# Kernel tuning notes

Measured on AMD Instinct MI355X. Metric: run time of the kernel, lower is better.

Reference implementation:

```python
import jax, jax.numpy as jnp
import numpy as np

K = 16                 # hardcoded k in KL_divergence default
TYPICAL_CRLB = 0.15 * 100 / 10   # = 1.5, sigma used in KL divergence


def setup_inputs() -> dict:
    key = jax.random.key(0)
    k1, k2 = jax.random.split(key)
    N = 8192
    ch1 = jax.random.normal(k1, (N, 2), dtype=jnp.float32)
    ch2 = jax.random.normal(k2, (N, 2), dtype=jnp.float32)
    # Polynomial layer parameters, exactly as in __init__ (identity-ish map)
    M1 = jnp.array([[0.0, 0.0], [1.0, 0.0]], dtype=jnp.float32)
    M2 = jnp.array([[0.0, 1.0], [0.0, 0.0]], dtype=jnp.float32)
    return {"ch1": ch1, "ch2": ch2, "M1": M1, "M2": M2}


def _polynomial(x, M1, M2):
    # out[:,0] = sum_ij M1[i,j] * x1^i * x2^j ; out[:,1] analog with M2 (m=2)
    x1, x2 = x[:, 0], x[:, 1]
    pi = jnp.stack([jnp.ones_like(x1), x1], axis=1)          # [N,2] -> x1^i
    pj = jnp.stack([jnp.ones_like(x2), x2], axis=1)          # [N,2] -> x2^j
    B = pi[:, :, None] * pj[:, None, :]                      # [N,2,2] basis x1^i*x2^j
    y1 = jnp.einsum('nij,ij->n', B, M1)
    y2 = jnp.einsum('nij,ij->n', B, M2)
    return jnp.stack([y1, y2], axis=1)                       # [N,2]


def reference(ch1, ch2, M1, M2):
    N = ch1.shape[0]
    ch2m = _polynomial(ch2, M1, M2)

    # --- KNN ---
    diff = ch1[None, :, :] - ch2m[:, None, :]                # [N2, N1, 2]
    distances = diff * diff                                  # squared per-coord dists
    abs_distances = jnp.sum(distances, axis=2)               # [N2, N1]
    # top_k of negated transposed distances: for each ch1 point, k nearest ch2m
    _, idx = jax.lax.top_k(-abs_distances.T, K)              # [N1, K] indices into ch2 axis
    # Faithful reproduction of the original index construction:
    # idx is flattened row-major ([N,K]); indx1 flattens a [K,N] arange-broadcast,
    # so the second coordinate at flat position t is t % N.
    flat_a = idx.reshape(-1)                                 # [N*K] indexes axis 0 (ch2)
    flat_b = jnp.tile(jnp.arange(N), K)                      # [N*K] indexes axis 1 (ch1)
    knn = distances[flat_a, flat_b].reshape(K, N, 2)         # [K, N, 2]

    # --- KL divergence ---
    sigma2 = TYPICAL_CRLB
    D_KL = 0.5 * jnp.sum(knn / (sigma2 ** 2), axis=2)        # [K, N]

    # --- Rel entropy ---
    expD = jnp.sum(jnp.exp(-D_KL), axis=0) / N               # [N]
    mask = expD != 0.0                                       # tf boolean_mask of nonzeros
    safe = jnp.where(mask, expD, 1.0)
    return -jnp.sum(jnp.where(mask, jnp.log(safe), 0.0))
```

## Files before the change

kernel.cpp:

```cpp
#include <hip/hip_runtime.h>
#include <math.h>
#include <stdint.h>

#define K_NN 16
#define NPTS 8192
#define HALF (NPTS / 2)
#define WPB 16

__global__ __launch_bounds__(1024) void k1_knn(const float* __restrict__ ch1,
                                               const float* __restrict__ ch2,
                                               const float* __restrict__ M1,
                                               const float* __restrict__ M2,
                                               int* __restrict__ midx,
                                               float* __restrict__ out) {
    __shared__ float2 sh[HALF];

    const int tid  = threadIdx.x;
    const int lane = tid & 63;
    const int w    = tid >> 6;
    const int qg   = blockIdx.x * WPB + w;

    if (blockIdx.x == 0 && tid == 0) out[0] = 0.0f;

    const float q0 = ch1[2 * qg + 0];
    const float q1 = ch1[2 * qg + 1];

    const float a0 = M1[0], a1 = M1[1], a2 = M1[2], a3 = M1[3];
    const float b0 = M2[0], b1 = M2[1], b2 = M2[2], b3 = M2[3];

    const float4* __restrict__ g4 = (const float4*)ch2;

    unsigned key = 0xFFFFFFFFu;
    unsigned kth = 0xFFFFFFFFu;

    for (int pass = 0; pass < 2; ++pass) {
        __syncthreads();
#pragma unroll
        for (int e = 0; e < (HALF / 2) / 1024; ++e) {
            float4 v = g4[pass * (HALF / 2) + e * 1024 + tid];
            float px0 = a0 + a1 * v.y + v.x * (a2 + a3 * v.y);
            float py0 = b0 + b1 * v.y + v.x * (b2 + b3 * v.y);
            float px1 = a0 + a1 * v.w + v.z * (a2 + a3 * v.w);
            float py1 = b0 + b1 * v.w + v.z * (b2 + b3 * v.w);
            ((float4*)sh)[e * 1024 + tid] = make_float4(px0, py0, px1, py1);
        }
        __syncthreads();

        const float4* s4 = (const float4*)sh;
        float4 c = s4[lane];

        for (int t = 0; t < HALF / 128; ++t) {
            float4 cn = s4[(((t + 1) & (HALF / 128 - 1)) * 64) + lane];
            int base = pass * HALF + (t * 64 + lane) * 2;
            float dx0 = q0 - c.x, dy0 = q1 - c.y;
            float dx1 = q0 - c.z, dy1 = q1 - c.w;
            float nd0 = dx0 * dx0 + dy0 * dy0;
            float nd1 = dx1 * dx1 + dy1 * dy1;
            unsigned nk0 = (__float_as_uint(nd0) & 0xFFFFE000u) | (unsigned)base;
            unsigned nk1 = (__float_as_uint(nd1) & 0xFFFFE000u) | (unsigned)(base + 1);

            unsigned long long m = __ballot(nk0 < kth);
            while (m) {
                int l = __ffsll(m) - 1;
                unsigned snk = (unsigned)__builtin_amdgcn_readlane((int)nk0, l);
                unsigned up = (unsigned)__builtin_amdgcn_update_dpp(
                    0, (int)key, 0x111, 0xF, 0xF, false);
                bool c1 = snk < key;
                unsigned nv = (snk < up) ? up : snk;
                key = c1 ? nv : key;
                kth = (unsigned)__builtin_amdgcn_readlane((int)key, 15);
                m &= m - 1;
                m &= __ballot(nk0 < kth);
            }

            m = __ballot(nk1 < kth);
            while (m) {
                int l = __ffsll(m) - 1;
                unsigned snk = (unsigned)__builtin_amdgcn_readlane((int)nk1, l);
                unsigned up = (unsigned)__builtin_amdgcn_update_dpp(
                    0, (int)key, 0x111, 0xF, 0xF, false);
                bool c1 = snk < key;
                unsigned nv = (snk < up) ? up : snk;
                key = c1 ? nv : key;
                kth = (unsigned)__builtin_amdgcn_readlane((int)key, 15);
                m &= m - 1;
                m &= __ballot(nk1 < kth);
            }

            c = cn;
        }
    }

    if (lane < K_NN)
        midx[qg * K_NN + lane] = (int)(key & 0x1FFFu);
}

__global__ __launch_bounds__(1024) void k3_final(const float* __restrict__ ch1,
                                                 const float* __restrict__ ch2,
                                                 const float* __restrict__ M1,
                                                 const float* __restrict__ M2,
                                                 const int* __restrict__ midx,
                                                 float* __restrict__ out, int N) {
    const float a0 = M1[0], a1 = M1[1], a2 = M1[2], a3 = M1[3];
    const float b0 = M2[0], b1 = M2[1], b2 = M2[2], b3 = M2[3];

    int t = blockIdx.x * 1024 + threadIdx.x;
    int n = t >> 4;
    int k = t & 15;
    int g = n >> 4;
    int r = n & 15;

    int j = k * (N / K_NN) + g;
    int a = midx[j * K_NN + r];
    float2 cp = ((const float2*)ch2)[a];
    float cx = a0 + a1 * cp.y + cp.x * (a2 + a3 * cp.y);
    float cy = b0 + b1 * cp.y + cp.x * (b2 + b3 * cp.y);
    float dx = ch1[2 * n + 0] - cx;
    float dy = ch1[2 * n + 1] - cy;
    float term = expf(-(dx * dx + dy * dy) * (1.0f / 4.5f));

#pragma unroll
    for (int off = 8; off; off >>= 1) term += __shfl_down(term, off, 16);

    float v = 0.0f;
    if (k == 0) {
        float expD = term / (float)N;
        v = (expD != 0.0f) ? logf(expD) : 0.0f;
    }
#pragma unroll
    for (int off = 32; off; off >>= 1) v += __shfl_down(v, off, 64);

    __shared__ float red[16];
    int lane = threadIdx.x & 63;
    int wv = threadIdx.x >> 6;
    if (lane == 0) red[wv] = v;
    __syncthreads();
    if (threadIdx.x == 0) {
        float s = 0.0f;
#pragma unroll
        for (int i = 0; i < 16; ++i) s += red[i];
        atomicAdd(out, -s);
    }
}

extern "C" void kernel_launch(void* const* d_in, const int* in_sizes, int n_in,
                              void* d_out, int out_size, void* d_ws, size_t ws_size,
                              hipStream_t stream) {
    const float* ch1 = (const float*)d_in[0];
    const float* ch2 = (const float*)d_in[1];
    const float* M1  = (const float*)d_in[2];
    const float* M2  = (const float*)d_in[3];
    float* out = (float*)d_out;
    const int N = in_sizes[0] / 2;

    int* midx = (int*)d_ws;

    k1_knn<<<N / WPB, 1024, 0, stream>>>(ch1, ch2, M1, M2, midx, out);

    k3_final<<<(N * K_NN) / 1024, 1024, 0, stream>>>(ch1, ch2, M1, M2, midx, out, N);
}
```

Measured before the change: 95.98 us.

## Replace brute-force KNN with uniform-grid spatial binning and ring search

Replaces the all-pairs distance scan with a 32x32 grid whose cell boundaries are normal-distribution quantiles. A single-block build kernel bins the transformed ch2 points, scans the counts into cell offsets and scatters the points into cell order. Each query wave then visits rings of cells outward and stops once the k-th key is within the ring margin, cutting distance evaluations from all points to a local neighbourhood. The costs are a serial single-block build launch and an extra kernel, and the quantile cell boundaries are tuned to Gaussian inputs (correct for any input but only efficient for this distribution).

```diff
diff --git a/kernel.cpp b/kernel.cpp
--- a/kernel.cpp
+++ b/kernel.cpp
@@ -4,92 +4,165 @@
 
 #define K_NN 16
 #define NPTS 8192
-#define HALF (NPTS / 2)
-#define WPB 16
-
-__global__ __launch_bounds__(1024) void k1_knn(const float* __restrict__ ch1,
-                                               const float* __restrict__ ch2,
-                                               const float* __restrict__ M1,
-                                               const float* __restrict__ M2,
-                                               int* __restrict__ midx,
-                                               float* __restrict__ out) {
-    __shared__ float2 sh[HALF];
-
-    const int tid  = threadIdx.x;
-    const int lane = tid & 63;
-    const int w    = tid >> 6;
-    const int qg   = blockIdx.x * WPB + w;
-
-    if (blockIdx.x == 0 && tid == 0) out[0] = 0.0f;
-
-    const float q0 = ch1[2 * qg + 0];
-    const float q1 = ch1[2 * qg + 1];
+#define G 32
+#define NC (G * G)
+
+static __device__ __constant__ float d_bt[33] = {
+    -3.4028235e38f,
+    -1.8627318f, -1.5341205f, -1.3180109f, -1.1503494f, -1.0100762f,
+    -0.8871466f, -0.7764218f, -0.6744898f, -0.5791322f, -0.4887764f,
+    -0.4022501f, -0.3186394f, -0.2372021f, -0.1573107f, -0.0784124f,
+     0.0f,
+     0.0784124f,  0.1573107f,  0.2372021f,  0.3186394f,  0.4022501f,
+     0.4887764f,  0.5791322f,  0.6744898f,  0.7764218f,  0.8871466f,
+     1.0100762f,  1.1503494f,  1.3180109f,  1.5341205f,  1.8627318f,
+     3.4028235e38f
+};
+
+__device__ __forceinline__ int bsearch5(const float* bt, float x) {
+    int c = 0;
+    c += (x >= bt[c + 16]) ? 16 : 0;
+    c += (x >= bt[c + 8])  ? 8  : 0;
+    c += (x >= bt[c + 4])  ? 4  : 0;
+    c += (x >= bt[c + 2])  ? 2  : 0;
+    c += (x >= bt[c + 1])  ? 1  : 0;
+    return c;
+}
+
+__global__ __launch_bounds__(1024) void kb_build(const float* __restrict__ ch2,
+                                                 const float* __restrict__ M1,
+                                                 const float* __restrict__ M2,
+                                                 float2* __restrict__ spts,
+                                                 int* __restrict__ sidx,
+                                                 int* __restrict__ cellStart,
+                                                 float* __restrict__ out) {
+    __shared__ int hist[NC];
+    __shared__ int scn[NC];
+    __shared__ float bt[33];
+    const int tid = threadIdx.x;
+    if (tid == 0) out[0] = 0.0f;
+    if (tid < 33) bt[tid] = d_bt[tid];
+    hist[tid] = 0;
+    __syncthreads();
 
     const float a0 = M1[0], a1 = M1[1], a2 = M1[2], a3 = M1[3];
     const float b0 = M2[0], b1 = M2[1], b2 = M2[2], b3 = M2[3];
 
-    const float4* __restrict__ g4 = (const float4*)ch2;
+    for (int i = tid; i < NPTS; i += 1024) {
+        float2 v = ((const float2*)ch2)[i];
+        float px = a0 + a1 * v.y + v.x * (a2 + a3 * v.y);
+        float py = b0 + b1 * v.y + v.x * (b2 + b3 * v.y);
+        int cx = bsearch5(bt, px);
+        int cy = bsearch5(bt, py);
+        atomicAdd(&hist[cy * G + cx], 1);
+    }
+    __syncthreads();
+
+    scn[tid] = hist[tid];
+    __syncthreads();
+    for (int off = 1; off < NC; off <<= 1) {
+        int t = scn[tid];
+        int u = (tid >= off) ? scn[tid - off] : 0;
+        __syncthreads();
+        scn[tid] = t + u;
+        __syncthreads();
+    }
+    int excl = scn[tid] - hist[tid];
+    cellStart[tid] = excl;
+    if (tid == NC - 1) cellStart[NC] = scn[tid];
+    __syncthreads();
+    hist[tid] = excl;
+    __syncthreads();
+
+    for (int i = tid; i < NPTS; i += 1024) {
+        float2 v = ((const float2*)ch2)[i];
+        float px = a0 + a1 * v.y + v.x * (a2 + a3 * v.y);
+        float py = b0 + b1 * v.y + v.x * (b2 + b3 * v.y);
+        int cx = bsearch5(bt, px);
+        int cy = bsearch5(bt, py);
+        int pos = atomicAdd(&hist[cy * G + cx], 1);
+        spts[pos] = make_float2(px, py);
+        sidx[pos] = i;
+    }
+}
+
+__global__ __launch_bounds__(256) void kq_query(const float* __restrict__ ch1,
+                                                const float2* __restrict__ spts,
+                                                const int* __restrict__ sidx,
+                                                const int* __restrict__ cellStart,
+                                                int* __restrict__ midx) {
+    __shared__ float bt[33];
+    const int tid = threadIdx.x;
+    if (tid < 33) bt[tid] = d_bt[tid];
+    __syncthreads();
+
+    const int lane = tid & 63;
+    const int qg = blockIdx.x * 4 + (tid >> 6);
+    const float qx = ch1[2 * qg + 0];
+    const float qy = ch1[2 * qg + 1];
+    const int cx = bsearch5(bt, qx);
+    const int cy = bsearch5(bt, qy);
 
     unsigned key = 0xFFFFFFFFu;
     unsigned kth = 0xFFFFFFFFu;
-
-    for (int pass = 0; pass < 2; ++pass) {
-        __syncthreads();
-#pragma unroll
-        for (int e = 0; e < (HALF / 2) / 1024; ++e) {
-            float4 v = g4[pass * (HALF / 2) + e * 1024 + tid];
-            float px0 = a0 + a1 * v.y + v.x * (a2 + a3 * v.y);
-            float py0 = b0 + b1 * v.y + v.x * (b2 + b3 * v.y);
-            float px1 = a0 + a1 * v.w + v.z * (a2 + a3 * v.w);
-            float py1 = b0 + b1 * v.w + v.z * (b2 + b3 * v.w);
-            ((float4*)sh)[e * 1024 + tid] = make_float4(px0, py0, px1, py1);
-        }
-        __syncthreads();
-
-        const float4* s4 = (const float4*)sh;
-        float4 c = s4[lane];
-
-        for (int t = 0; t < HALF / 128; ++t) {
-            float4 cn = s4[(((t + 1) & (HALF / 128 - 1)) * 64) + lane];
-            int base = pass * HALF + (t * 64 + lane) * 2;
-            float dx0 = q0 - c.x, dy0 = q1 - c.y;
-            float dx1 = q0 - c.z, dy1 = q1 - c.w;
-            float nd0 = dx0 * dx0 + dy0 * dy0;
-            float nd1 = dx1 * dx1 + dy1 * dy1;
-            unsigned nk0 = (__float_as_uint(nd0) & 0xFFFFE000u) | (unsigned)base;
-            unsigned nk1 = (__float_as_uint(nd1) & 0xFFFFE000u) | (unsigned)(base + 1);
-
-            unsigned long long m = __ballot(nk0 < kth);
-            while (m) {
-                int l = __ffsll(m) - 1;
-                unsigned snk = (unsigned)__builtin_amdgcn_readlane((int)nk0, l);
-                unsigned up = (unsigned)__builtin_amdgcn_update_dpp(
-                    0, (int)key, 0x111, 0xF, 0xF, false);
-                bool c1 = snk < key;
-                unsigned nv = (snk < up) ? up : snk;
-                key = c1 ? nv : key;
-                kth = (unsigned)__builtin_amdgcn_readlane((int)key, 15);
-                m &= m - 1;
-                m &= __ballot(nk0 < kth);
-            }
-
-            m = __ballot(nk1 < kth);
-            while (m) {
-                int l = __ffsll(m) - 1;
-                unsigned snk = (unsigned)__builtin_amdgcn_readlane((int)nk1, l);
-                unsigned up = (unsigned)__builtin_amdgcn_update_dpp(
-                    0, (int)key, 0x111, 0xF, 0xF, false);
-                bool c1 = snk < key;
-                unsigned nv = (snk < up) ? up : snk;
-                key = c1 ? nv : key;
-                kth = (unsigned)__builtin_amdgcn_readlane((int)key, 15);
-                m &= m - 1;
-                m &= __ballot(nk1 < kth);
-            }
-
-            c = cn;
-        }
-    }
+    unsigned thr = 0xFFFFFFFFu;
+
+#define SCAN_RANGE(ROW, CA, CB)                                               \
+    {                                                                         \
+        int st = cellStart[(ROW) * G + (CA)];                                 \
+        int en = cellStart[(ROW) * G + (CB) + 1];                             \
+        for (int base = st; base < en; base += 64) {                          \
+            int i = base + lane;                                              \
+            unsigned ndb = 0xFFFFFFFFu;                                       \
+            int si = 0x1FFF;                                                  \
+            if (i < en) {                                                     \
+                float2 p = spts[i];                                           \
+                si = sidx[i];                                                 \
+                float dx = qx - p.x, dy = qy - p.y;                           \
+                ndb = __float_as_uint(dx * dx + dy * dy);                     \
+            }                                                                 \
+            unsigned long long m = __ballot(ndb <= thr);                      \
+            while (m) {                                                       \
+                int l = __ffsll(m) - 1;                                       \
+                unsigned snd = (unsigned)__builtin_amdgcn_readlane((int)ndb, l); \
+                unsigned ssi = (unsigned)__builtin_amdgcn_readlane(si, l);    \
+                unsigned snk = (snd & 0xFFFFE000u) | ssi;                     \
+                if (snk < kth) {                                              \
+                    unsigned up = (unsigned)__builtin_amdgcn_update_dpp(      \
+                        0, (int)key, 0x111, 0xF, 0xF, false);  \
+                    bool c1 = snk < key;                                      \
+                    unsigned nv = (snk < up) ? up : snk;                      \
+                    key = c1 ? nv : key;                                      \
+                    kth = (unsigned)__builtin_amdgcn_readlane((int)key, 15);  \
+                    thr = kth | 0x1FFFu;                                      \
+                }                                                             \
+                m &= m - 1;                                                   \
+                m &= __ballot(ndb <= thr);                                    \
+            }                                                                 \
+        }                                                                     \
+    }
+
+    for (int r = 0; r <= 2 * G; ++r) {
+        int rlo = cy - r, rhi = cy + r;
+        int clo = max(cx - r, 0), chi = min(cx + r, G - 1);
+        if (rlo >= 0) SCAN_RANGE(rlo, clo, chi)
+        if (rhi <= G - 1 && r > 0) SCAN_RANGE(rhi, clo, chi)
+        int mlo = max(rlo + 1, 0), mhi = min(rhi - 1, G - 1);
+        if (cx - r >= 0)
+            for (int rr = mlo; rr <= mhi; ++rr) SCAN_RANGE(rr, cx - r, cx - r)
+        if (cx + r <= G - 1)
+            for (int rr = mlo; rr <= mhi; ++rr) SCAN_RANGE(rr, cx + r, cx + r)
+
+        float Lx = (cx - r <= 0)     ? -3.4028235e38f : bt[cx - r];
+        float Rx = (cx + r >= G - 1) ?  3.4028235e38f : bt[cx + r + 1];
+        float Ly = (cy - r <= 0)     ? -3.4028235e38f : bt[cy - r];
+        float Ry = (cy + r >= G - 1) ?  3.4028235e38f : bt[cy + r + 1];
+        float mg = fminf(fminf(qx - Lx, Rx - qx), fminf(qy - Ly, Ry - qy));
+        mg = fmaxf(mg, 0.0f);
+        float kd = __uint_as_float(kth & 0xFFFFE000u);
+        if (kd <= mg * mg) break;
+    }
+#undef SCAN_RANGE
 
     if (lane < K_NN)
         midx[qg * K_NN + lane] = (int)(key & 0x1FFFu);
@@ -153,9 +226,15 @@
     float* out = (float*)d_out;
     const int N = in_sizes[0] / 2;
 
-    int* midx = (int*)d_ws;
-
-    k1_knn<<<N / WPB, 1024, 0, stream>>>(ch1, ch2, M1, M2, midx, out);
+    char* ws = (char*)d_ws;
+    float2* spts     = (float2*)ws;
+    int*    midx     = (int*)(ws + 65536);
+    int*    sidx     = (int*)(ws + 65536 + 524288);
+    int*    cellStart= (int*)(ws + 65536 + 524288 + 32768);
+
+    kb_build<<<1, 1024, 0, stream>>>(ch2, M1, M2, spts, sidx, cellStart, out);
+
+    kq_query<<<N / 4, 256, 0, stream>>>(ch1, spts, sidx, cellStart, midx);
 
     k3_final<<<(N * K_NN) / 1024, 1024, 0, stream>>>(ch1, ch2, M1, M2, midx, out, N);
 }
```

Result: slower. 155.0 us (+61.5%).

## Replace brute-force KNN scan with y-band bucketed search and pruning

Applied to the files above, without the earlier changes.

Adds a single-block build kernel that bins transformed ch2 points into 32 horizontal bands whose boundaries are normal-distribution quantiles, then counting-sorts them. The query kernel scans the query's own band first and expands outward, stopping once a band's vertical distance exceeds the current k-th best. This replaces scanning all 8192 candidates per query. The band boundaries are tuned for standard-normal inputs, so the pruning only helps on similar data, and the extra serial build kernel adds latency.

```diff
diff --git a/kernel.cpp b/kernel.cpp
--- a/kernel.cpp
+++ b/kernel.cpp
@@ -4,92 +4,171 @@
 
 #define K_NN 16
 #define NPTS 8192
-#define HALF (NPTS / 2)
-#define WPB 16
-
-__global__ __launch_bounds__(1024) void k1_knn(const float* __restrict__ ch1,
-                                               const float* __restrict__ ch2,
-                                               const float* __restrict__ M1,
-                                               const float* __restrict__ M2,
-                                               int* __restrict__ midx,
-                                               float* __restrict__ out) {
-    __shared__ float2 sh[HALF];
+#define NR 32
+
+static __device__ __constant__ float d_bt[33] = {
+    -3.4028235e38f,
+    -1.8627318f, -1.5341205f, -1.3180109f, -1.1503494f, -1.0100762f,
+    -0.8871466f, -0.7764218f, -0.6744898f, -0.5791322f, -0.4887764f,
+    -0.4022501f, -0.3186394f, -0.2372021f, -0.1573107f, -0.0784124f,
+     0.0f,
+     0.0784124f,  0.1573107f,  0.2372021f,  0.3186394f,  0.4022501f,
+     0.4887764f,  0.5791322f,  0.6744898f,  0.7764218f,  0.8871466f,
+     1.0100762f,  1.1503494f,  1.3180109f,  1.5341205f,  1.8627318f,
+     3.4028235e38f
+};
+
+__device__ __forceinline__ int rowOf(const float* bt, float y) {
+    int c = 0;
+    c += (y >= bt[c + 16]) ? 16 : 0;
+    c += (y >= bt[c + 8])  ? 8  : 0;
+    c += (y >= bt[c + 4])  ? 4  : 0;
+    c += (y >= bt[c + 2])  ? 2  : 0;
+    c += (y >= bt[c + 1])  ? 1  : 0;
+    return c;
+}
+
+__global__ __launch_bounds__(1024) void kb_build(const float* __restrict__ ch2,
+                                                 const float* __restrict__ M1,
+                                                 const float* __restrict__ M2,
+                                                 float2* __restrict__ spts,
+                                                 int* __restrict__ sidx,
+                                                 int* __restrict__ rowStart,
+                                                 float* __restrict__ out) {
+    __shared__ int h[NR];
+    __shared__ int offs[NR];
+    __shared__ float bt[33];
+    const int tid = threadIdx.x;
+    if (tid == 0) out[0] = 0.0f;
+    if (tid < 33) bt[tid] = d_bt[tid];
+    if (tid < NR) h[tid] = 0;
+    __syncthreads();
+
+    const float a0 = M1[0], a1 = M1[1], a2 = M1[2], a3 = M1[3];
+    const float b0 = M2[0], b1 = M2[1], b2 = M2[2], b3 = M2[3];
+
+    for (int i = tid; i < NPTS; i += 1024) {
+        float2 v = ((const float2*)ch2)[i];
+        float py = b0 + b1 * v.y + v.x * (b2 + b3 * v.y);
+        atomicAdd(&h[rowOf(bt, py)], 1);
+    }
+    __syncthreads();
+
+    if (tid == 0) {
+        int run = 0;
+        for (int r = 0; r < NR; ++r) { offs[r] = run; rowStart[r] = run; run += h[r]; }
+        rowStart[NR] = run;
+    }
+    __syncthreads();
+
+    for (int i = tid; i < NPTS; i += 1024) {
+        float2 v = ((const float2*)ch2)[i];
+        float px = a0 + a1 * v.y + v.x * (a2 + a3 * v.y);
+        float py = b0 + b1 * v.y + v.x * (b2 + b3 * v.y);
+        int pos = atomicAdd(&offs[rowOf(bt, py)], 1);
+        spts[pos] = make_float2(px, py);
+        sidx[pos] = i;
+    }
+}
+
+__global__ __launch_bounds__(1024) void kq_query(const float* __restrict__ ch1,
+                                                 const float2* __restrict__ spts,
+                                                 const int* __restrict__ gsidx,
+                                                 const int* __restrict__ rowStart,
+                                                 int* __restrict__ midx) {
+    __shared__ float2 shp[NPTS];
 
     const int tid  = threadIdx.x;
     const int lane = tid & 63;
     const int w    = tid >> 6;
-    const int qg   = blockIdx.x * WPB + w;
-
-    if (blockIdx.x == 0 && tid == 0) out[0] = 0.0f;
-
-    const float q0 = ch1[2 * qg + 0];
-    const float q1 = ch1[2 * qg + 1];
-
-    const float a0 = M1[0], a1 = M1[1], a2 = M1[2], a3 = M1[3];
-    const float b0 = M2[0], b1 = M2[1], b2 = M2[2], b3 = M2[3];
-
-    const float4* __restrict__ g4 = (const float4*)ch2;
+    const int qg   = blockIdx.x * 16 + w;
+
+#pragma unroll
+    for (int e = 0; e < 4; ++e)
+        ((float4*)shp)[e * 1024 + tid] = ((const float4*)spts)[e * 1024 + tid];
+
+    int btb = __float_as_int(d_bt[lane < 33 ? lane : 0]);
+    int rsv = rowStart[lane < 33 ? lane : 0];
+    __syncthreads();
+
+    const float qx = ch1[2 * qg + 0];
+    const float qy = ch1[2 * qg + 1];
+
+    int own = rowOf(d_bt, qy);
 
     unsigned key = 0xFFFFFFFFu;
-    unsigned kth = 0xFFFFFFFFu;
-
-    for (int pass = 0; pass < 2; ++pass) {
-        __syncthreads();
-#pragma unroll
-        for (int e = 0; e < (HALF / 2) / 1024; ++e) {
-            float4 v = g4[pass * (HALF / 2) + e * 1024 + tid];
-            float px0 = a0 + a1 * v.y + v.x * (a2 + a3 * v.y);
-            float py0 = b0 + b1 * v.y + v.x * (b2 + b3 * v.y);
-            float px1 = a0 + a1 * v.w + v.z * (a2 + a3 * v.w);
-            float py1 = b0 + b1 * v.w + v.z * (b2 + b3 * v.w);
-            ((float4*)sh)[e * 1024 + tid] = make_float4(px0, py0, px1, py1);
+    unsigned thr = 0xFFFFFFFFu;
+    bool first = true;
+
+#define SCAN_ROW(R)                                                            \
+    {                                                                          \
+        int lo = __builtin_amdgcn_readlane(rsv, (R));                          \
+        int hi = __builtin_amdgcn_readlane(rsv, (R) + 1);                      \
+        for (int base = lo; base < hi; base += 64) {                           \
+            int i = base + lane;                                               \
+            bool act = i < hi;                                                 \
+            int ii = act ? i : (hi - 1);                                       \
+            float2 p = shp[ii];                                                \
+            int si = gsidx[ii];                                                \
+            float dx = qx - p.x, dy = qy - p.y;                                \
+            unsigned u = act ? __float_as_uint(dx * dx + dy * dy)              \
+                             : 0xFFFFFFFFu;                                    \
+            if (first) {                                                       \
+                first = false;                                                 \
+                unsigned mn = min(u, (unsigned)__shfl_xor((int)u, 1, 64));     \
+                mn = min(mn, (unsigned)__shfl_xor((int)mn, 2, 64));            \
+                unsigned mx = mn;                                              \
+                mx = max(mx, (unsigned)__shfl_xor((int)mx, 4, 64));            \
+                mx = max(mx, (unsigned)__shfl_xor((int)mx, 8, 64));            \
+                mx = max(mx, (unsigned)__shfl_xor((int)mx, 16, 64));           \
+                mx = max(mx, (unsigned)__shfl_xor((int)mx, 32, 64));           \
+                thr = mx | 0x1FFFu;                                            \
+            }                                                                  \
+            unsigned nk = (u & 0xFFFFE000u) | (unsigned)si;                    \
+            unsigned long long m = __ballot(u <= thr);                         \
+            while (m) {                                                        \
+                int l = __ffsll(m) - 1;                                        \
+                m &= m - 1;                                                    \
+                unsigned snk = (unsigned)__builtin_amdgcn_readlane((int)nk, l);\
+                unsigned up = (unsigned)__builtin_amdgcn_update_dpp(           \
+                    0, (int)key, 0x111, 0xF, 0xF, false);       \
+                bool c1 = snk < key;                                           \
+                unsigned nv = (snk < up) ? up : snk;                           \
+                key = c1 ? nv : key;                                           \
+            }                                                                  \
+            thr = (unsigned)__builtin_amdgcn_readlane((int)key, 15) | 0x1FFFu; \
+        }                                                                      \
+    }
+
+    SCAN_ROW(own)
+
+    bool loDone = false, hiDone = false;
+    for (int d = 1; d < NR; ++d) {
+        unsigned kthT = thr & 0xFFFFE000u;
+        int rlo = own - d, rhi = own + d;
+        if (!loDone) {
+            if (rlo < 0) loDone = true;
+            else {
+                float band = qy - __uint_as_float(
+                    __builtin_amdgcn_readlane(btb, rlo + 1));
+                unsigned bb = __float_as_uint(band * band) & 0xFFFFE000u;
+                if (bb > kthT) loDone = true;
+                else SCAN_ROW(rlo)
+            }
         }
-        __syncthreads();
-
-        const float4* s4 = (const float4*)sh;
-        float4 c = s4[lane];
-
-        for (int t = 0; t < HALF / 128; ++t) {
-            float4 cn = s4[(((t + 1) & (HALF / 128 - 1)) * 64) + lane];
-            int base = pass * HALF + (t * 64 + lane) * 2;
-            float dx0 = q0 - c.x, dy0 = q1 - c.y;
-            float dx1 = q0 - c.z, dy1 = q1 - c.w;
-            float nd0 = dx0 * dx0 + dy0 * dy0;
-            float nd1 = dx1 * dx1 + dy1 * dy1;
-            unsigned nk0 = (__float_as_uint(nd0) & 0xFFFFE000u) | (unsigned)base;
-            unsigned nk1 = (__float_as_uint(nd1) & 0xFFFFE000u) | (unsigned)(base + 1);
-
-            unsigned long long m = __ballot(nk0 < kth);
-            while (m) {
-                int l = __ffsll(m) - 1;
-                unsigned snk = (unsigned)__builtin_amdgcn_readlane((int)nk0, l);
-                unsigned up = (unsigned)__builtin_amdgcn_update_dpp(
-                    0, (int)key, 0x111, 0xF, 0xF, false);
-                bool c1 = snk < key;
-                unsigned nv = (snk < up) ? up : snk;
-                key = c1 ? nv : key;
-                kth = (unsigned)__builtin_amdgcn_readlane((int)key, 15);
-                m &= m - 1;
-                m &= __ballot(nk0 < kth);
+        if (!hiDone) {
+            if (rhi > NR - 1) hiDone = true;
+            else {
+                float band = __uint_as_float(
+                    __builtin_amdgcn_readlane(btb, rhi)) - qy;
+                unsigned bb = __float_as_uint(band * band) & 0xFFFFE000u;
+                if (bb > (thr & 0xFFFFE000u)) hiDone = true;
+                else SCAN_ROW(rhi)
             }
-
-            m = __ballot(nk1 < kth);
-            while (m) {
-                int l = __ffsll(m) - 1;
-                unsigned snk = (unsigned)__builtin_amdgcn_readlane((int)nk1, l);
-                unsigned up = (unsigned)__builtin_amdgcn_update_dpp(
-                    0, (int)key, 0x111, 0xF, 0xF, false);
-                bool c1 = snk < key;
-                unsigned nv = (snk < up) ? up : snk;
-                key = c1 ? nv : key;
-                kth = (unsigned)__builtin_amdgcn_readlane((int)key, 15);
-                m &= m - 1;
-                m &= __ballot(nk1 < kth);
-            }
-
-            c = cn;
         }
-    }
+        if (loDone && hiDone) break;
+    }
+#undef SCAN_ROW
 
     if (lane < K_NN)
         midx[qg * K_NN + lane] = (int)(key & 0x1FFFu);
@@ -153,9 +232,15 @@
     float* out = (float*)d_out;
     const int N = in_sizes[0] / 2;
 
-    int* midx = (int*)d_ws;
-
-    k1_knn<<<N / WPB, 1024, 0, stream>>>(ch1, ch2, M1, M2, midx, out);
+    char* ws = (char*)d_ws;
+    float2* spts     = (float2*)ws;
+    int*    sidx     = (int*)(ws + 65536);
+    int*    rowStart = (int*)(ws + 65536 + 32768);
+    int*    midx     = (int*)(ws + 65536 + 32768 + 256);
+
+    kb_build<<<1, 1024, 0, stream>>>(ch2, M1, M2, spts, sidx, rowStart, out);
+
+    kq_query<<<N / 16, 1024, 0, stream>>>(ch1, spts, sidx, rowStart, midx);
 
     k3_final<<<(N * K_NN) / 1024, 1024, 0, stream>>>(ch1, ch2, M1, M2, midx, out, N);
 }
```

After: 100.8 us. 1.05x slower.
